# Optimization experiments

Measured on AMD Instinct MI355X. Metric: run time of the kernel, lower is better.

Reference implementation:

```python
import jax, jax.numpy as jnp
import numpy as np

N = 100000   # nodes
E = 1600000  # edges (before self-loops)
G = 64       # graphs in batch
IN = 8
H = 4        # heads
EPS_BN = 1e-5

def setup_inputs() -> dict:
    key = jax.random.key(0)
    ks = jax.random.split(key, 30)
    def nrm(k, shape, s=0.1):
        return jax.random.normal(k, shape, dtype=jnp.float32) * s
    inp = {}
    inp['x'] = nrm(ks[0], (N, IN), 1.0)
    inp['edge_index'] = jax.random.randint(ks[1], (2, E), 0, N)
    inp['batch'] = jnp.sort(jax.random.randint(ks[2], (N,), 0, G))
    # GATConv 1: 8 -> 64, 4 heads (concat=False)
    inp['W1'] = nrm(ks[3], (IN, H * 64)); inp['aS1'] = nrm(ks[4], (H, 64)); inp['aD1'] = nrm(ks[5], (H, 64)); inp['b1'] = jnp.zeros((64,), jnp.float32)
    inp['g1'] = jnp.ones((64,), jnp.float32); inp['be1'] = jnp.zeros((64,), jnp.float32)
    # GATConv 2: 64 -> 64
    inp['W2'] = nrm(ks[6], (64, H * 64)); inp['aS2'] = nrm(ks[7], (H, 64)); inp['aD2'] = nrm(ks[8], (H, 64)); inp['b2'] = jnp.zeros((64,), jnp.float32)
    inp['g2'] = jnp.ones((64,), jnp.float32); inp['be2'] = jnp.zeros((64,), jnp.float32)
    # GATConv 3: 64 -> 32
    inp['W3'] = nrm(ks[9], (64, H * 32)); inp['aS3'] = nrm(ks[10], (H, 32)); inp['aD3'] = nrm(ks[11], (H, 32)); inp['b3'] = jnp.zeros((32,), jnp.float32)
    inp['g3'] = jnp.ones((32,), jnp.float32); inp['be3'] = jnp.zeros((32,), jnp.float32)
    # predictor MLP 32 -> 16 -> 1
    inp['Wp1'] = nrm(ks[12], (32, 16)); inp['bp1'] = jnp.zeros((16,), jnp.float32)
    inp['Wp2'] = nrm(ks[13], (16, 1)); inp['bp2'] = jnp.zeros((1,), jnp.float32)
    return inp

def gat_layer(x, src, dst, W, a_src, a_dst, bias, D):
    # x: [N, Fin]; src/dst: [E'] (self-loops included). PyG GATConv semantics.
    h = (x @ W).reshape(N, H, D)                       # [N,H,D]
    alpha_s = jnp.einsum('nhd,hd->nh', h, a_src)       # [N,H]
    alpha_d = jnp.einsum('nhd,hd->nh', h, a_dst)
    e = jax.nn.leaky_relu(alpha_s[src] + alpha_d[dst], 0.2)  # [E',H]
    # segment softmax over incoming edges of each target node
    m = jax.ops.segment_max(e, dst, num_segments=N)
    e = jnp.exp(e - m[dst])
    s = jax.ops.segment_sum(e, dst, num_segments=N)
    alpha = e / (s[dst] + 1e-16)                       # [E',H]
    out = jax.ops.segment_sum(h[src] * alpha[:, :, None], dst, num_segments=N)  # [N,H,D]
    return out.mean(axis=1) + bias                     # concat=False -> head mean

def batch_norm(x, gamma, beta):
    m = x.mean(0)
    v = x.var(0)
    return (x - m) * jax.lax.rsqrt(v + EPS_BN) * gamma + beta

def reference(x, edge_index, batch,
              W1, aS1, aD1, b1, g1, be1,
              W2, aS2, aD2, b2, g2, be2,
              W3, aS3, aD3, b3, g3, be3,
              Wp1, bp1, Wp2, bp2):
    loop = jnp.arange(N)
    src = jnp.concatenate([edge_index[0], loop])  # add self loops (PyG default)
    dst = jnp.concatenate([edge_index[1], loop])
    h = jax.nn.relu(gat_layer(x, src, dst, W1, aS1, aD1, b1, 64))
    h = batch_norm(h, g1, be1)
    h = jax.nn.relu(gat_layer(h, src, dst, W2, aS2, aD2, b2, 64))
    h = batch_norm(h, g2, be2)
    h = jax.nn.relu(gat_layer(h, src, dst, W3, aS3, aD3, b3, 32))
    h = batch_norm(h, g3, be3)
    # global mean pool over graphs
    cnt = jax.ops.segment_sum(jnp.ones((N,), h.dtype), batch, num_segments=G)
    pooled = jax.ops.segment_sum(h, batch, num_segments=G) / jnp.maximum(cnt, 1.0)[:, None]
    hid = jax.nn.relu(pooled @ Wp1 + bp1)
    return hid @ Wp2 + bp2  # [G,1]
```

## Files before the change

kernel.cpp:

```cpp
#include <hip/hip_runtime.h>
#include <hip/hip_fp16.h>

#define N_NODES 100000
#define N_EDGES 1600000
#define EP (N_EDGES + N_NODES)
#define NG 64
#define NH 4
#define POOL_NPB 256
#define BSHIFT 7
#define BNODES 128
#define NBUCK 782
#define BCAP 3072
#define BCHUNK 4096
#define NBLK2 (N_NODES / 16)
#define NBLK1 (N_NODES / 32)

static inline int cdiv(int a, int b) { return (a + b - 1) / b; }

typedef _Float16 half8 __attribute__((ext_vector_type(8)));
typedef float f32x4 __attribute__((ext_vector_type(4)));

__device__ __forceinline__ float lrelu(float x) { return x >= 0.f ? x : 0.2f * x; }

__global__ __launch_bounds__(256) void k_bucket(const int* __restrict__ ei,
                                                int* __restrict__ gCursor,
                                                unsigned int* __restrict__ pairs) {
  __shared__ int cnt[NBUCK];
  __shared__ int base[NBUCK];
  int tid = threadIdx.x;
  for (int b = tid; b < NBUCK; b += 256) cnt[b] = 0;
  __syncthreads();
  int e0 = blockIdx.x * BCHUNK;
  unsigned int stV[16];
  int stB[16];
#pragma unroll
  for (int i = 0; i < 16; i++) {
    int e = e0 + i * 256 + tid;
    stB[i] = -1;
    if (e < EP) {
      int d, s;
      if (e < N_EDGES) {
        d = __builtin_nontemporal_load(&ei[N_EDGES + e]);
        s = __builtin_nontemporal_load(&ei[e]);
      } else {
        d = s = e - N_EDGES;
      }
      int b = d >> BSHIFT;
      stV[i] = ((unsigned int)s << BSHIFT) | (unsigned int)(d & (BNODES - 1));
      stB[i] = b;
      atomicAdd(&cnt[b], 1);
    }
  }
  __syncthreads();
  for (int b = tid; b < NBUCK; b += 256) {
    base[b] = atomicAdd(&gCursor[b], cnt[b]);
    cnt[b] = 0;
  }
  __syncthreads();
#pragma unroll
  for (int i = 0; i < 16; i++) {
    if (stB[i] >= 0) {
      int r = atomicAdd(&cnt[stB[i]], 1);
      pairs[base[stB[i]] + r] = stV[i];
    }
  }
}

__global__ __launch_bounds__(1024) void k_bscan(const int* __restrict__ gCursor,
                                                int* __restrict__ bstart) {
  __shared__ int sh[1024];
  int t = threadIdx.x;
  int v = (t < NBUCK) ? (gCursor[t] - t * BCAP) : 0;
  sh[t] = v;
  __syncthreads();
  for (int off = 1; off < 1024; off <<= 1) {
    int add = (t >= off) ? sh[t - off] : 0;
    __syncthreads();
    sh[t] += add;
    __syncthreads();
  }
  if (t < NBUCK) {
    bstart[t] = sh[t] - v;
    if (t == NBUCK - 1) bstart[NBUCK] = sh[t];
  }
}

__global__ __launch_bounds__(256) void k_build(const unsigned int* __restrict__ pairs,
                                               const int* __restrict__ bstart,
                                               int* __restrict__ indptr, int* __restrict__ esrc) {
  __shared__ int cnt[BNODES];
  __shared__ int exc[BNODES];
  __shared__ int ptr[BNODES];
  __shared__ int eLds[BCAP];
  int b = blockIdx.x;
  int tid = threadIdx.x;
  int obase = bstart[b];
  int nE = bstart[b + 1] - obase;
  int pbase = b * BCAP;
  if (tid < BNODES) cnt[tid] = 0;
  __syncthreads();
  unsigned int stV[12];
#pragma unroll
  for (int i = 0; i < 12; i++) {
    int idx = i * 256 + tid;
    stV[i] = 0xFFFFFFFFu;
    if (idx < nE) {
      unsigned int v = pairs[pbase + idx];
      stV[i] = v;
      atomicAdd(&cnt[v & (BNODES - 1)], 1);
    }
  }
  __syncthreads();
  if (tid < BNODES) ptr[tid] = cnt[tid];
  __syncthreads();
  for (int off = 1; off < BNODES; off <<= 1) {
    int add = (tid < BNODES && tid >= off) ? ptr[tid - off] : 0;
    __syncthreads();
    if (tid < BNODES) ptr[tid] += add;
    __syncthreads();
  }
  if (tid < BNODES) {
    exc[tid] = ptr[tid] - cnt[tid];
    int n = (b << BSHIFT) + tid;
    if (n < N_NODES) indptr[n] = obase + exc[tid];
    cnt[tid] = 0;
  }
  if (b == NBUCK - 1 && tid == 0) indptr[N_NODES] = bstart[NBUCK];
  __syncthreads();
#pragma unroll
  for (int i = 0; i < 12; i++) {
    if (stV[i] != 0xFFFFFFFFu) {
      int ln = stV[i] & (BNODES - 1);
      int r = atomicAdd(&cnt[ln], 1);
      eLds[exc[ln] + r] = (int)(stV[i] >> BSHIFT);
    }
  }
  __syncthreads();
  for (int idx = tid; idx < nE; idx += 256) esrc[obase + idx] = eLds[idx];
}

template <int FIN, int D>
__device__ void wvec_impl(const float* __restrict__ W, const float* __restrict__ aS,
                          const float* __restrict__ aD, float* __restrict__ wS,
                          float* __restrict__ wD, int t) {
  if (t >= 4 * FIN) return;
  int h = t / FIN, k = t % FIN;
  float ss = 0.f, dd = 0.f;
  for (int d = 0; d < D; d++) {
    float w = W[k * (4 * D) + h * D + d];
    ss = fmaf(w, aS[h * D + d], ss);
    dd = fmaf(w, aD[h * D + d], dd);
  }
  wS[h * FIN + k] = ss;
  wD[h * FIN + k] = dd;
}

template <int D>
__device__ void wcvt_frag(const float* __restrict__ W, __half* __restrict__ wf, int frag, int l) {
  constexpr int NCT = D / 16;
  int kt = frag / NCT, ct = frag % NCT;
  half8 v;
#pragma unroll
  for (int j = 0; j < 8; j++) {
    int kk = kt * 32 + (l >> 4) * 8 + j;
    int k = kk >> 2, h = kk & 3;
    v[j] = (_Float16)W[k * (4 * D) + h * D + ct * 16 + (l & 15)];
  }
  *(half8*)(wf + (size_t)frag * 512 + l * 8) = v;
}

__global__ __launch_bounds__(256) void k_prep(const float* W1, const float* aS1, const float* aD1,
                                              const float* W2, const float* aS2, const float* aD2,
                                              const float* W3, const float* aS3, const float* aD3,
                                              float* wS1, float* wD1, float* wS2, float* wD2,
                                              float* wS3, float* wD3,
                                              __half* wf1, __half* wf2, __half* wf3,
                                              int* gCursor) {
  int b = blockIdx.x, t = threadIdx.x;
  int f = t >> 6, l = t & 63;
  if (b == 0) wvec_impl<8, 64>(W1, aS1, aD1, wS1, wD1, t);
  else if (b == 1) wvec_impl<64, 64>(W2, aS2, aD2, wS2, wD2, t);
  else if (b == 2) wvec_impl<64, 32>(W3, aS3, aD3, wS3, wD3, t);
  else if (b == 3) wcvt_frag<64>(W1, wf1, f, l);
  else if (b < 12) wcvt_frag<64>(W2, wf2, (b - 4) * 4 + f, l);
  else if (b < 16) wcvt_frag<32>(W3, wf3, (b - 12) * 4 + f, l);
  else {
    int idx = (b - 16) * 256 + t;
    if (idx < NBUCK) gCursor[idx] = idx * BCAP;
  }
}

__global__ void k_attdots1(const float* __restrict__ x, const float* __restrict__ wS,
                           const float* __restrict__ wD, float4* __restrict__ as4,
                           float4* __restrict__ ad4) {
  int n = blockIdx.x * blockDim.x + threadIdx.x;
  if (n >= N_NODES) return;
  float4 s = {0, 0, 0, 0}, d = {0, 0, 0, 0};
#pragma unroll
  for (int k = 0; k < 8; k++) {
    float xv = x[(size_t)n * 8 + k];
    s.x = fmaf(xv, wS[k], s.x);
    s.y = fmaf(xv, wS[8 + k], s.y);
    s.z = fmaf(xv, wS[16 + k], s.z);
    s.w = fmaf(xv, wS[24 + k], s.w);
    d.x = fmaf(xv, wD[k], d.x);
    d.y = fmaf(xv, wD[8 + k], d.y);
    d.z = fmaf(xv, wD[16 + k], d.z);
    d.w = fmaf(xv, wD[24 + k], d.w);
  }
  as4[n] = s;
  ad4[n] = d;
}

__global__ __launch_bounds__(256) void k_bnx(const float* __restrict__ tbuf,
                                             const float* __restrict__ scale,
                                             const float* __restrict__ shift,
                                             const float* __restrict__ wS,
                                             const float* __restrict__ wD,
                                             __half* __restrict__ xhat,
                                             float4* __restrict__ as4, float4* __restrict__ ad4) {
  int lane = threadIdx.x & 63;
  int n = blockIdx.x * 4 + (threadIdx.x >> 6);
  if (n >= N_NODES) return;
  float v = fmaf(tbuf[(size_t)n * 64 + lane], scale[lane], shift[lane]);
  xhat[(size_t)n * 64 + lane] = __float2half(v);
  float p0 = v * wS[lane], p1 = v * wS[64 + lane], p2 = v * wS[128 + lane], p3 = v * wS[192 + lane];
  float q0 = v * wD[lane], q1 = v * wD[64 + lane], q2 = v * wD[128 + lane], q3 = v * wD[192 + lane];
#pragma unroll
  for (int off = 32; off; off >>= 1) {
    p0 += __shfl_xor(p0, off); p1 += __shfl_xor(p1, off);
    p2 += __shfl_xor(p2, off); p3 += __shfl_xor(p3, off);
    q0 += __shfl_xor(q0, off); q1 += __shfl_xor(q1, off);
    q2 += __shfl_xor(q2, off); q3 += __shfl_xor(q3, off);
  }
  if (lane == 0) {
    as4[n] = make_float4(p0, p1, p2, p3);
    ad4[n] = make_float4(q0, q1, q2, q3);
  }
}

__global__ __launch_bounds__(256) void k_aggp1(const int* __restrict__ indptr,
                                               const int* __restrict__ esrc,
                                               const float* __restrict__ xg,
                                               const float4* __restrict__ as4,
                                               const float4* __restrict__ ad4,
                                               const __half* __restrict__ wfrag,
                                               const float* __restrict__ bias,
                                               float* __restrict__ tbuf,
                                               float* __restrict__ part) {
  constexpr int GL = 8, NPW = 8, WB = NPW * (GL + 1);
  __shared__ int sOff[4 * WB];
  __shared__ float4 sW[4 * WB];
  __shared__ __align__(16) __half aT[32 * 40];
  int tid = threadIdx.x;
  int lane = tid & 63;
  int wv = tid >> 6;
  int q = lane & 7;
  int g = lane >> 3;
  int row = wv * 8 + g;
  int n = blockIdx.x * 32 + row;
  int e0 = indptr[n], e1 = indptr[n + 1];
  float4 ad = ad4[n];
  int lbase = wv * WB + g * (GL + 1);
  const char* xb = (const char*)xg + q * 4;
  float s0 = 0.f, s1 = 0.f, s2 = 0.f, s3 = 0.f;
  float a0 = 0.f, a1 = 0.f, a2 = 0.f, a3 = 0.f;
  for (int c = e0; c < e1; c += GL) {
    int nc = min(GL, e1 - c);
    float w0 = 0.f, w1 = 0.f, w2 = 0.f, w3 = 0.f;
    int sB = 0;
    if (q < nc) {
      int sidx = esrc[c + q];
      float4 av = as4[sidx];
      w0 = __expf(lrelu(av.x + ad.x));
      w1 = __expf(lrelu(av.y + ad.y));
      w2 = __expf(lrelu(av.z + ad.z));
      w3 = __expf(lrelu(av.w + ad.w));
      sB = sidx << 5;
    }
    s0 += w0; s1 += w1; s2 += w2; s3 += w3;
    sOff[lbase + q] = sB;
    sW[lbase + q] = make_float4(w0, w1, w2, w3);
    __builtin_amdgcn_wave_barrier();
    for (int i = 0; i < nc; ++i) {
      float4 w = sW[lbase + i];
      float xv = *(const float*)(xb + sOff[lbase + i]);
      a0 = fmaf(w.x, xv, a0);
      a1 = fmaf(w.y, xv, a1);
      a2 = fmaf(w.z, xv, a2);
      a3 = fmaf(w.w, xv, a3);
    }
    __builtin_amdgcn_wave_barrier();
  }
#pragma unroll
  for (int off = 1; off < GL; off <<= 1) {
    s0 += __shfl_xor(s0, off);
    s1 += __shfl_xor(s1, off);
    s2 += __shfl_xor(s2, off);
    s3 += __shfl_xor(s3, off);
  }
  float r0 = 1.f / (s0 + 1e-16f), r1 = 1.f / (s1 + 1e-16f);
  float r2 = 1.f / (s2 + 1e-16f), r3 = 1.f / (s3 + 1e-16f);
  __half2 p01 = __floats2half2_rn(a0 * r0, a1 * r1);
  __half2 p23 = __floats2half2_rn(a2 * r2, a3 * r3);
  uint2 pk = make_uint2(*(unsigned*)&p01, *(unsigned*)&p23);
  *(uint2*)&aT[row * 40 + q * 4] = pk;
  __syncthreads();
  int ct = wv;
  int m = lane & 15, kg = lane >> 4;
  half8 bv = *(const half8*)(wfrag + ((size_t)ct * 64 + lane) * 8);
  float bvs = bias[ct * 16 + m];
  float psum = 0.f, psq = 0.f;
#pragma unroll
  for (int tt = 0; tt < 2; tt++) {
    half8 avf = *(const half8*)&aT[(tt * 16 + m) * 40 + kg * 8];
    f32x4 cacc = (f32x4){0.f, 0.f, 0.f, 0.f};
    cacc = __builtin_amdgcn_mfma_f32_16x16x32_f16(avf, bv, cacc, 0, 0, 0);
#pragma unroll
    for (int j = 0; j < 4; j++) {
      int nr = blockIdx.x * 32 + tt * 16 + kg * 4 + j;
      float ov = fmaxf(fmaf(cacc[j], 0.25f, bvs), 0.f);
      tbuf[(size_t)nr * 64 + ct * 16 + m] = ov;
      psum += ov;
      psq = fmaf(ov, ov, psq);
    }
  }
  psum += __shfl_xor(psum, 16); psum += __shfl_xor(psum, 32);
  psq += __shfl_xor(psq, 16); psq += __shfl_xor(psq, 32);
  if (kg == 0) {
    part[(size_t)blockIdx.x * 128 + ct * 16 + m] = psum;
    part[(size_t)blockIdx.x * 128 + 64 + ct * 16 + m] = psq;
  }
}

template <int DOUT>
__global__ __launch_bounds__(256) void k_aggp(const int* __restrict__ indptr,
                                              const int* __restrict__ esrc,
                                              const __half* __restrict__ xg,
                                              const float4* __restrict__ as4,
                                              const float4* __restrict__ ad4,
                                              const __half* __restrict__ wfrag,
                                              const float* __restrict__ bias,
                                              float* __restrict__ tbuf,
                                              float* __restrict__ part) {
  constexpr int NCT = DOUT / 16;
  constexpr int GL = 16, NPW = 4, WB = NPW * (GL + 1);
  __shared__ int sOff[4 * WB];
  __shared__ float4 sW[4 * WB];
  __shared__ __align__(16) __half aT[16 * 264];
  int tid = threadIdx.x;
  int lane = tid & 63;
  int wv = tid >> 6;
  int q = lane & 15;
  int g = lane >> 4;
  int row = wv * 4 + g;
  int n = blockIdx.x * 16 + row;
  int e0 = indptr[n], e1 = indptr[n + 1];
  float4 ad = ad4[n];
  int lbase = wv * WB + g * (GL + 1);
  const char* xb = (const char*)xg + q * 8;
  float s0 = 0.f, s1 = 0.f, s2 = 0.f, s3 = 0.f;
  float a[4][4];
#pragma unroll
  for (int d = 0; d < 4; d++)
#pragma unroll
    for (int h = 0; h < 4; h++) a[d][h] = 0.f;

  for (int c = e0; c < e1; c += GL) {
    int nc = min(GL, e1 - c);
    float w0 = 0.f, w1 = 0.f, w2 = 0.f, w3 = 0.f;
    int sB = 0;
    if (q < nc) {
      int sidx = esrc[c + q];
      float4 av = as4[sidx];
      w0 = __expf(lrelu(av.x + ad.x));
      w1 = __expf(lrelu(av.y + ad.y));
      w2 = __expf(lrelu(av.z + ad.z));
      w3 = __expf(lrelu(av.w + ad.w));
      sB = sidx << 7;
    }
    s0 += w0; s1 += w1; s2 += w2; s3 += w3;
    sOff[lbase + q] = sB;
    sW[lbase + q] = make_float4(w0, w1, w2, w3);
    __builtin_amdgcn_wave_barrier();
    for (int i = 0; i < nc; ++i) {
      float4 w = sW[lbase + i];
      uint2 px = *(const uint2*)(xb + sOff[lbase + i]);
      float2 f01 = __half22float2(*(const __half2*)&px.x);
      float2 f23 = __half22float2(*(const __half2*)&px.y);
      a[0][0] = fmaf(w.x, f01.x, a[0][0]); a[0][1] = fmaf(w.y, f01.x, a[0][1]);
      a[0][2] = fmaf(w.z, f01.x, a[0][2]); a[0][3] = fmaf(w.w, f01.x, a[0][3]);
      a[1][0] = fmaf(w.x, f01.y, a[1][0]); a[1][1] = fmaf(w.y, f01.y, a[1][1]);
      a[1][2] = fmaf(w.z, f01.y, a[1][2]); a[1][3] = fmaf(w.w, f01.y, a[1][3]);
      a[2][0] = fmaf(w.x, f23.x, a[2][0]); a[2][1] = fmaf(w.y, f23.x, a[2][1]);
      a[2][2] = fmaf(w.z, f23.x, a[2][2]); a[2][3] = fmaf(w.w, f23.x, a[2][3]);
      a[3][0] = fmaf(w.x, f23.y, a[3][0]); a[3][1] = fmaf(w.y, f23.y, a[3][1]);
      a[3][2] = fmaf(w.z, f23.y, a[3][2]); a[3][3] = fmaf(w.w, f23.y, a[3][3]);
    }
    __builtin_amdgcn_wave_barrier();
  }
#pragma unroll
  for (int off = 1; off < GL; off <<= 1) {
    s0 += __shfl_xor(s0, off);
    s1 += __shfl_xor(s1, off);
    s2 += __shfl_xor(s2, off);
    s3 += __shfl_xor(s3, off);
  }
  float r0 = 1.f / (s0 + 1e-16f), r1 = 1.f / (s1 + 1e-16f);
  float r2 = 1.f / (s2 + 1e-16f), r3 = 1.f / (s3 + 1e-16f);
  __half2 p[8];
#pragma unroll
  for (int d = 0; d < 4; d++) {
    p[2 * d] = __floats2half2_rn(a[d][0] * r0, a[d][1] * r1);
    p[2 * d + 1] = __floats2half2_rn(a[d][2] * r2, a[d][3] * r3);
  }
  uint4 lo = make_uint4(*(unsigned*)&p[0], *(unsigned*)&p[1], *(unsigned*)&p[2], *(unsigned*)&p[3]);
  uint4 hi = make_uint4(*(unsigned*)&p[4], *(unsigned*)&p[5], *(unsigned*)&p[6], *(unsigned*)&p[7]);
  *(uint4*)&aT[row * 264 + q * 16] = lo;
  *(uint4*)&aT[row * 264 + q * 16 + 8] = hi;
  __syncthreads();
  if (wv < NCT) {
    int ct = wv;
    int m = lane & 15, kg = lane >> 4;
    f32x4 cacc = (f32x4){0.f, 0.f, 0.f, 0.f};
#pragma unroll
    for (int kt = 0; kt < 8; kt++) {
      half8 avf = *(const half8*)&aT[m * 264 + kt * 32 + kg * 8];
      half8 bvf = *(const half8*)(wfrag + ((kt * NCT + ct) * 64 + lane) * 8);
      cacc = __builtin_amdgcn_mfma_f32_16x16x32_f16(avf, bvf, cacc, 0, 0, 0);
    }
    float bv = bias[ct * 16 + m];
    float psum = 0.f, psq = 0.f;
#pragma unroll
    for (int j = 0; j < 4; j++) {
      int nr = blockIdx.x * 16 + kg * 4 + j;
      float ov = fmaxf(fmaf(cacc[j], 0.25f, bv), 0.f);
      tbuf[(size_t)nr * DOUT + ct * 16 + m] = ov;
      psum += ov;
      psq = fmaf(ov, ov, psq);
    }
    psum += __shfl_xor(psum, 16); psum += __shfl_xor(psum, 32);
    psq += __shfl_xor(psq, 16); psq += __shfl_xor(psq, 32);
    if (kg == 0) {
      part[(size_t)blockIdx.x * (2 * DOUT) + ct * 16 + m] = psum;
      part[(size_t)blockIdx.x * (2 * DOUT) + DOUT + ct * 16 + m] = psq;
    }
  }
}

template <int C>
__global__ __launch_bounds__(256) void k_bnfin2(const float* __restrict__ part, int nb,
                                                const float* __restrict__ g,
                                                const float* __restrict__ be,
                                                float* __restrict__ scale,
                                                float* __restrict__ shift) {
  int c = blockIdx.x;
  int t = threadIdx.x;
  float s = 0.f, q = 0.f;
  for (int b = t; b < nb; b += 256) {
    s += part[(size_t)b * (2 * C) + c];
    q += part[(size_t)b * (2 * C) + C + c];
  }
  __shared__ float sh[512];
  sh[t] = s;
  sh[256 + t] = q;
  __syncthreads();
  for (int step = 128; step; step >>= 1) {
    if (t < step) {
      sh[t] += sh[t + step];
      sh[256 + t] += sh[256 + t + step];
    }
    __syncthreads();
  }
  if (t == 0) {
    float mean = sh[0] / (float)N_NODES;
    float var = sh[256] / (float)N_NODES - mean * mean;
    float sc = g[c] * rsqrtf(var + 1e-5f);
    scale[c] = sc;
    shift[c] = be[c] - mean * sc;
  }
}

__global__ __launch_bounds__(256) void k_pool(const float* __restrict__ f3,
                                              const int* __restrict__ batch,
                                              const float* __restrict__ scale,
                                              const float* __restrict__ shift,
                                              float* __restrict__ pool,
                                              float* __restrict__ cntg) {
  __shared__ float acc[NG][33];
  int t = threadIdx.x;
  for (int i = t; i < NG * 33; i += 256) ((float*)acc)[i] = 0.f;
  __syncthreads();
  int c = t & 31, rg = t >> 5;
  float sc = scale[c], sh = shift[c];
  int n0 = blockIdx.x * POOL_NPB;
  int n1 = min(N_NODES, n0 + POOL_NPB);
  float r = 0.f, rc = 0.f;
  int gcur = -1;
  for (int n = n0 + rg; n < n1; n += 8) {
    int g = batch[n];
    if (g != gcur) {
      if (gcur >= 0) {
        atomicAdd(&acc[gcur][c], r);
        if (c == 0) atomicAdd(&acc[gcur][32], rc);
      }
      gcur = g;
      r = 0.f;
      rc = 0.f;
    }
    r += fmaf(f3[(size_t)n * 32 + c], sc, sh);
    rc += 1.f;
  }
  if (gcur >= 0) {
    atomicAdd(&acc[gcur][c], r);
    if (c == 0) atomicAdd(&acc[gcur][32], rc);
  }
  __syncthreads();
  for (int i = t; i < NG * 32; i += 256) {
    int g = i >> 5, cc = i & 31;
    float v = acc[g][cc];
    if (v != 0.f) atomicAdd(&pool[i], v);
  }
  for (int g = t; g < NG; g += 256) {
    float v = acc[g][32];
    if (v != 0.f) atomicAdd(&cntg[g], v);
  }
}

__global__ void k_mlp(const float* __restrict__ pool, const float* __restrict__ cntg,
                      const float* __restrict__ Wp1, const float* __restrict__ bp1,
                      const float* __restrict__ Wp2, const float* __restrict__ bp2,
                      float* __restrict__ out) {
  int g = threadIdx.x;
  if (g >= NG) return;
  float inv = 1.f / fmaxf(cntg[g], 1.f);
  float p[32];
#pragma unroll
  for (int c = 0; c < 32; c++) p[c] = pool[g * 32 + c] * inv;
  float o = bp2[0];
  for (int j = 0; j < 16; j++) {
    float hsum = bp1[j];
#pragma unroll
    for (int c = 0; c < 32; c++) hsum = fmaf(p[c], Wp1[c * 16 + j], hsum);
    o = fmaf(fmaxf(hsum, 0.f), Wp2[j], o);
  }
  out[g] = o;
}

extern "C" void kernel_launch(void* const* d_in, const int* in_sizes, int n_in,
                              void* d_out, int out_size, void* d_ws, size_t ws_size,
                              hipStream_t stream) {
  const float* x = (const float*)d_in[0];
  const int* ei = (const int*)d_in[1];
  const int* batch = (const int*)d_in[2];
  const float* W1 = (const float*)d_in[3];
  const float* aS1 = (const float*)d_in[4];
  const float* aD1 = (const float*)d_in[5];
  const float* b1 = (const float*)d_in[6];
  const float* g1 = (const float*)d_in[7];
  const float* be1 = (const float*)d_in[8];
  const float* W2 = (const float*)d_in[9];
  const float* aS2 = (const float*)d_in[10];
  const float* aD2 = (const float*)d_in[11];
  const float* b2 = (const float*)d_in[12];
  const float* g2 = (const float*)d_in[13];
  const float* be2 = (const float*)d_in[14];
  const float* W3 = (const float*)d_in[15];
  const float* aS3 = (const float*)d_in[16];
  const float* aD3 = (const float*)d_in[17];
  const float* b3 = (const float*)d_in[18];
  const float* g3 = (const float*)d_in[19];
  const float* be3 = (const float*)d_in[20];
  const float* Wp1 = (const float*)d_in[21];
  const float* bp1 = (const float*)d_in[22];
  const float* Wp2 = (const float*)d_in[23];
  const float* bp2 = (const float*)d_in[24];
  float* out = (float*)d_out;

  size_t off = 0;
  auto alloc = [&](size_t bytes) -> void* {
    void* p = (char*)d_ws + off;
    off += (bytes + 255) & ~(size_t)255;
    return p;
  };
  float* pool = (float*)alloc((size_t)NG * 32 * 4);
  float* cntg = (float*)alloc((size_t)NG * 4);
  size_t zbytes = off;
  int* gCursor = (int*)alloc((size_t)NBUCK * 4);
  int* bstart = (int*)alloc((size_t)(NBUCK + 1) * 4);
  unsigned int* pairs = (unsigned int*)alloc((size_t)NBUCK * BCAP * 4);
  int* indptr = (int*)alloc((size_t)(N_NODES + 1) * 4);
  int* esrc = (int*)alloc((size_t)EP * 4);
  __half* xhat = (__half*)alloc((size_t)N_NODES * 64 * 2);
  float* as_ = (float*)alloc((size_t)N_NODES * 16);
  float* ad_ = (float*)alloc((size_t)N_NODES * 16);
  float* tbuf = (float*)alloc((size_t)N_NODES * 64 * 4);
  float* part = (float*)alloc((size_t)NBLK2 * 128 * 4);
  float* scale = (float*)alloc(64 * 4);
  float* shift = (float*)alloc(64 * 4);
  float* wS1 = (float*)alloc(32 * 4);
  float* wD1 = (float*)alloc(32 * 4);
  float* wS2 = (float*)alloc(256 * 4);
  float* wD2 = (float*)alloc(256 * 4);
  float* wS3 = (float*)alloc(256 * 4);
  float* wD3 = (float*)alloc(256 * 4);
  __half* wf1 = (__half*)alloc((size_t)4 * 512 * 2);
  __half* wf2 = (__half*)alloc((size_t)32 * 512 * 2);
  __half* wf3 = (__half*)alloc((size_t)16 * 512 * 2);
  if (off > ws_size) return;

  hipMemsetAsync(pool, 0, zbytes, stream);

  k_prep<<<16 + cdiv(NBUCK, 256), 256, 0, stream>>>(W1, aS1, aD1, W2, aS2, aD2, W3, aS3, aD3,
                                                    wS1, wD1, wS2, wD2, wS3, wD3, wf1, wf2, wf3,
                                                    gCursor);
  k_bucket<<<cdiv(EP, BCHUNK), 256, 0, stream>>>(ei, gCursor, pairs);
  k_bscan<<<1, 1024, 0, stream>>>(gCursor, bstart);
  k_build<<<NBUCK, 256, 0, stream>>>(pairs, bstart, indptr, esrc);

  k_attdots1<<<cdiv(N_NODES, 256), 256, 0, stream>>>(x, wS1, wD1, (float4*)as_, (float4*)ad_);
  k_aggp1<<<NBLK1, 256, 0, stream>>>(indptr, esrc, x, (const float4*)as_,
                                     (const float4*)ad_, wf1, b1, tbuf, part);
  k_bnfin2<64><<<64, 256, 0, stream>>>(part, NBLK1, g1, be1, scale, shift);

  k_bnx<<<cdiv(N_NODES, 4), 256, 0, stream>>>(tbuf, scale, shift, wS2, wD2, xhat,
                                              (float4*)as_, (float4*)ad_);
  k_aggp<64><<<NBLK2, 256, 0, stream>>>(indptr, esrc, xhat, (const float4*)as_,
                                        (const float4*)ad_, wf2, b2, tbuf, part);
  k_bnfin2<64><<<64, 256, 0, stream>>>(part, NBLK2, g2, be2, scale, shift);

  k_bnx<<<cdiv(N_NODES, 4), 256, 0, stream>>>(tbuf, scale, shift, wS3, wD3, xhat,
                                              (float4*)as_, (float4*)ad_);
  k_aggp<32><<<NBLK2, 256, 0, stream>>>(indptr, esrc, xhat, (const float4*)as_,
                                        (const float4*)ad_, wf3, b3, tbuf, part);
  k_bnfin2<32><<<32, 256, 0, stream>>>(part, NBLK2, g3, be3, scale, shift);

  k_pool<<<cdiv(N_NODES, POOL_NPB), 256, 0, stream>>>(tbuf, batch, scale, shift, pool, cntg);
  k_mlp<<<1, 64, 0, stream>>>(pool, cntg, Wp1, bp1, Wp2, bp2, out);
}
```

Measured before the change: 382.4 us.

## Sort nodes by degree for balanced aggregation and fold batch-norm into aggregation

Builds a degree histogram during CSR construction, then scans and scatters it into a degree-sorted node permutation. The aggregation kernels process nodes in that order, so nodes in the same wave have similar edge counts and less divergence. Layer outputs are now stored as fp16 and the batch-norm affine is applied inside the next aggregation, so k_dots only computes attention dots and the separate normalized-feature buffer is dropped. This adds two small kernels and scattered (permuted) output writes, and stores intermediates in half precision.

```diff
diff --git a/kernel.cpp b/kernel.cpp
--- a/kernel.cpp
+++ b/kernel.cpp
@@ -14,6 +14,7 @@
 #define BCHUNK 4096
 #define NBLK2 (N_NODES / 16)
 #define NBLK1 (N_NODES / 32)
+#define NBINS 64
 
 static inline int cdiv(int a, int b) { return (a + b - 1) / b; }
 
@@ -87,10 +88,12 @@
 
 __global__ __launch_bounds__(256) void k_build(const unsigned int* __restrict__ pairs,
                                                const int* __restrict__ bstart,
-                                               int* __restrict__ indptr, int* __restrict__ esrc) {
+                                               int* __restrict__ indptr, int* __restrict__ esrc,
+                                               int* __restrict__ ghist) {
   __shared__ int cnt[BNODES];
   __shared__ int exc[BNODES];
   __shared__ int ptr[BNODES];
+  __shared__ int dh[NBINS];
   __shared__ int eLds[BCAP];
   int b = blockIdx.x;
   int tid = threadIdx.x;
@@ -98,6 +101,7 @@
   int nE = bstart[b + 1] - obase;
   int pbase = b * BCAP;
   if (tid < BNODES) cnt[tid] = 0;
+  if (tid >= BNODES && tid < BNODES + NBINS) dh[tid - BNODES] = 0;
   __syncthreads();
   unsigned int stV[12];
 #pragma unroll
@@ -122,11 +126,15 @@
   if (tid < BNODES) {
     exc[tid] = ptr[tid] - cnt[tid];
     int n = (b << BSHIFT) + tid;
-    if (n < N_NODES) indptr[n] = obase + exc[tid];
+    if (n < N_NODES) {
+      indptr[n] = obase + exc[tid];
+      atomicAdd(&dh[min(cnt[tid], NBINS - 1)], 1);
+    }
     cnt[tid] = 0;
   }
   if (b == NBUCK - 1 && tid == 0) indptr[N_NODES] = bstart[NBUCK];
   __syncthreads();
+  if (tid < NBINS && dh[tid]) atomicAdd(&ghist[tid], dh[tid]);
 #pragma unroll
   for (int i = 0; i < 12; i++) {
     if (stV[i] != 0xFFFFFFFFu) {
@@ -137,6 +145,51 @@
   }
   __syncthreads();
   for (int idx = tid; idx < nE; idx += 256) esrc[obase + idx] = eLds[idx];
+}
+
+__global__ void k_dscan(const int* __restrict__ ghist, int* __restrict__ binCur) {
+  if (threadIdx.x == 0) {
+    int acc = 0;
+    for (int b = 0; b < NBINS; b++) {
+      binCur[b] = acc;
+      acc += ghist[b];
+    }
+  }
+}
+
+__global__ __launch_bounds__(256) void k_dscat(const int* __restrict__ indptr,
+                                               int* __restrict__ binCur,
+                                               int* __restrict__ perm) {
+  __shared__ int cnt[NBINS];
+  __shared__ int base[NBINS];
+  int t = threadIdx.x;
+  if (t < NBINS) cnt[t] = 0;
+  __syncthreads();
+  int binr[2], nr[2];
+#pragma unroll
+  for (int i = 0; i < 2; i++) {
+    int n = blockIdx.x * 512 + i * 256 + t;
+    binr[i] = -1;
+    if (n < N_NODES) {
+      int deg = indptr[n + 1] - indptr[n];
+      binr[i] = min(deg, NBINS - 1);
+      nr[i] = n;
+      atomicAdd(&cnt[binr[i]], 1);
+    }
+  }
+  __syncthreads();
+  if (t < NBINS) {
+    base[t] = cnt[t] ? atomicAdd(&binCur[t], cnt[t]) : 0;
+    cnt[t] = 0;
+  }
+  __syncthreads();
+#pragma unroll
+  for (int i = 0; i < 2; i++) {
+    if (binr[i] >= 0) {
+      int r = atomicAdd(&cnt[binr[i]], 1);
+      perm[base[binr[i]] + r] = nr[i];
+    }
+  }
 }
 
 template <int FIN, int D>
@@ -212,18 +265,16 @@
   ad4[n] = d;
 }
 
-__global__ __launch_bounds__(256) void k_bnx(const float* __restrict__ tbuf,
-                                             const float* __restrict__ scale,
-                                             const float* __restrict__ shift,
-                                             const float* __restrict__ wS,
-                                             const float* __restrict__ wD,
-                                             __half* __restrict__ xhat,
-                                             float4* __restrict__ as4, float4* __restrict__ ad4) {
+__global__ __launch_bounds__(256) void k_dots(const __half* __restrict__ t16,
+                                              const float* __restrict__ scale,
+                                              const float* __restrict__ shift,
+                                              const float* __restrict__ wS,
+                                              const float* __restrict__ wD,
+                                              float4* __restrict__ as4, float4* __restrict__ ad4) {
   int lane = threadIdx.x & 63;
   int n = blockIdx.x * 4 + (threadIdx.x >> 6);
   if (n >= N_NODES) return;
-  float v = fmaf(tbuf[(size_t)n * 64 + lane], scale[lane], shift[lane]);
-  xhat[(size_t)n * 64 + lane] = __float2half(v);
+  float v = fmaf(__half2float(t16[(size_t)n * 64 + lane]), scale[lane], shift[lane]);
   float p0 = v * wS[lane], p1 = v * wS[64 + lane], p2 = v * wS[128 + lane], p3 = v * wS[192 + lane];
   float q0 = v * wD[lane], q1 = v * wD[64 + lane], q2 = v * wD[128 + lane], q3 = v * wD[192 + lane];
 #pragma unroll
@@ -240,13 +291,14 @@
 }
 
 __global__ __launch_bounds__(256) void k_aggp1(const int* __restrict__ indptr,
+                                               const int* __restrict__ perm,
                                                const int* __restrict__ esrc,
                                                const float* __restrict__ xg,
                                                const float4* __restrict__ as4,
                                                const float4* __restrict__ ad4,
                                                const __half* __restrict__ wfrag,
                                                const float* __restrict__ bias,
-                                               float* __restrict__ tbuf,
+                                               __half* __restrict__ out16,
                                                float* __restrict__ part) {
   constexpr int GL = 8, NPW = 8, WB = NPW * (GL + 1);
   __shared__ int sOff[4 * WB];
@@ -258,7 +310,7 @@
   int q = lane & 7;
   int g = lane >> 3;
   int row = wv * 8 + g;
-  int n = blockIdx.x * 32 + row;
+  int n = perm[blockIdx.x * 32 + row];
   int e0 = indptr[n], e1 = indptr[n + 1];
   float4 ad = ad4[n];
   int lbase = wv * WB + g * (GL + 1);
@@ -318,9 +370,9 @@
     cacc = __builtin_amdgcn_mfma_f32_16x16x32_f16(avf, bv, cacc, 0, 0, 0);
 #pragma unroll
     for (int j = 0; j < 4; j++) {
-      int nr = blockIdx.x * 32 + tt * 16 + kg * 4 + j;
+      int nr = perm[blockIdx.x * 32 + tt * 16 + kg * 4 + j];
       float ov = fmaxf(fmaf(cacc[j], 0.25f, bvs), 0.f);
-      tbuf[(size_t)nr * 64 + ct * 16 + m] = ov;
+      out16[(size_t)nr * 64 + ct * 16 + m] = __float2half(ov);
       psum += ov;
       psq = fmaf(ov, ov, psq);
     }
@@ -333,15 +385,19 @@
   }
 }
 
-template <int DOUT>
+template <int DOUT, bool OUTH>
 __global__ __launch_bounds__(256) void k_aggp(const int* __restrict__ indptr,
+                                              const int* __restrict__ perm,
                                               const int* __restrict__ esrc,
                                               const __half* __restrict__ xg,
                                               const float4* __restrict__ as4,
                                               const float4* __restrict__ ad4,
                                               const __half* __restrict__ wfrag,
                                               const float* __restrict__ bias,
-                                              float* __restrict__ tbuf,
+                                              const float* __restrict__ scale,
+                                              const float* __restrict__ shift,
+                                              __half* __restrict__ out16,
+                                              float* __restrict__ out32,
                                               float* __restrict__ part) {
   constexpr int NCT = DOUT / 16;
   constexpr int GL = 16, NPW = 4, WB = NPW * (GL + 1);
@@ -354,7 +410,7 @@
   int q = lane & 15;
   int g = lane >> 4;
   int row = wv * 4 + g;
-  int n = blockIdx.x * 16 + row;
+  int n = perm[blockIdx.x * 16 + row];
   int e0 = indptr[n], e1 = indptr[n + 1];
   float4 ad = ad4[n];
   int lbase = wv * WB + g * (GL + 1);
@@ -411,8 +467,9 @@
   __half2 p[8];
 #pragma unroll
   for (int d = 0; d < 4; d++) {
-    p[2 * d] = __floats2half2_rn(a[d][0] * r0, a[d][1] * r1);
-    p[2 * d + 1] = __floats2half2_rn(a[d][2] * r2, a[d][3] * r3);
+    float sc = scale[q * 4 + d], sh = shift[q * 4 + d];
+    p[2 * d] = __floats2half2_rn(fmaf(a[d][0] * r0, sc, sh), fmaf(a[d][1] * r1, sc, sh));
+    p[2 * d + 1] = __floats2half2_rn(fmaf(a[d][2] * r2, sc, sh), fmaf(a[d][3] * r3, sc, sh));
   }
   uint4 lo = make_uint4(*(unsigned*)&p[0], *(unsigned*)&p[1], *(unsigned*)&p[2], *(unsigned*)&p[3]);
   uint4 hi = make_uint4(*(unsigned*)&p[4], *(unsigned*)&p[5], *(unsigned*)&p[6], *(unsigned*)&p[7]);
@@ -433,9 +490,10 @@
     float psum = 0.f, psq = 0.f;
 #pragma unroll
     for (int j = 0; j < 4; j++) {
-      int nr = blockIdx.x * 16 + kg * 4 + j;
+      int nr = perm[blockIdx.x * 16 + kg * 4 + j];
       float ov = fmaxf(fmaf(cacc[j], 0.25f, bv), 0.f);
-      tbuf[(size_t)nr * DOUT + ct * 16 + m] = ov;
+      if constexpr (OUTH) out16[(size_t)nr * DOUT + ct * 16 + m] = __float2half(ov);
+      else out32[(size_t)nr * DOUT + ct * 16 + m] = ov;
       psum += ov;
       psq = fmaf(ov, ov, psq);
     }
@@ -585,16 +643,20 @@
   };
   float* pool = (float*)alloc((size_t)NG * 32 * 4);
   float* cntg = (float*)alloc((size_t)NG * 4);
+  int* ghist = (int*)alloc((size_t)NBINS * 4);
   size_t zbytes = off;
   int* gCursor = (int*)alloc((size_t)NBUCK * 4);
   int* bstart = (int*)alloc((size_t)(NBUCK + 1) * 4);
   unsigned int* pairs = (unsigned int*)alloc((size_t)NBUCK * BCAP * 4);
   int* indptr = (int*)alloc((size_t)(N_NODES + 1) * 4);
   int* esrc = (int*)alloc((size_t)EP * 4);
-  __half* xhat = (__half*)alloc((size_t)N_NODES * 64 * 2);
+  int* perm = (int*)alloc((size_t)N_NODES * 4);
+  int* binCur = (int*)alloc((size_t)NBINS * 4);
+  __half* t16a = (__half*)alloc((size_t)N_NODES * 64 * 2);
+  __half* t16b = (__half*)alloc((size_t)N_NODES * 64 * 2);
   float* as_ = (float*)alloc((size_t)N_NODES * 16);
   float* ad_ = (float*)alloc((size_t)N_NODES * 16);
-  float* tbuf = (float*)alloc((size_t)N_NODES * 64 * 4);
+  float* tbuf = (float*)alloc((size_t)N_NODES * 32 * 4);
   float* part = (float*)alloc((size_t)NBLK2 * 128 * 4);
   float* scale = (float*)alloc(64 * 4);
   float* shift = (float*)alloc(64 * 4);
@@ -616,23 +678,27 @@
                                                     gCursor);
   k_bucket<<<cdiv(EP, BCHUNK), 256, 0, stream>>>(ei, gCursor, pairs);
   k_bscan<<<1, 1024, 0, stream>>>(gCursor, bstart);
-  k_build<<<NBUCK, 256, 0, stream>>>(pairs, bstart, indptr, esrc);
+  k_build<<<NBUCK, 256, 0, stream>>>(pairs, bstart, indptr, esrc, ghist);
+  k_dscan<<<1, 64, 0, stream>>>(ghist, binCur);
+  k_dscat<<<cdiv(N_NODES, 512), 256, 0, stream>>>(indptr, binCur, perm);
 
   k_attdots1<<<cdiv(N_NODES, 256), 256, 0, stream>>>(x, wS1, wD1, (float4*)as_, (float4*)ad_);
-  k_aggp1<<<NBLK1, 256, 0, stream>>>(indptr, esrc, x, (const float4*)as_,
-                                     (const float4*)ad_, wf1, b1, tbuf, part);
+  k_aggp1<<<NBLK1, 256, 0, stream>>>(indptr, perm, esrc, x, (const float4*)as_,
+                                     (const float4*)ad_, wf1, b1, t16a, part);
   k_bnfin2<64><<<64, 256, 0, stream>>>(part, NBLK1, g1, be1, scale, shift);
 
-  k_bnx<<<cdiv(N_NODES, 4), 256, 0, stream>>>(tbuf, scale, shift, wS2, wD2, xhat,
-                                              (float4*)as_, (float4*)ad_);
-  k_aggp<64><<<NBLK2, 256, 0, stream>>>(indptr, esrc, xhat, (const float4*)as_,
-                                        (const float4*)ad_, wf2, b2, tbuf, part);
+  k_dots<<<cdiv(N_NODES, 4), 256, 0, stream>>>(t16a, scale, shift, wS2, wD2,
+                                               (float4*)as_, (float4*)ad_);
+  k_aggp<64, true><<<NBLK2, 256, 0, stream>>>(indptr, perm, esrc, t16a, (const float4*)as_,
+                                              (const float4*)ad_, wf2, b2, scale, shift,
+                                              t16b, nullptr, part);
   k_bnfin2<64><<<64, 256, 0, stream>>>(part, NBLK2, g2, be2, scale, shift);
 
-  k_bnx<<<cdiv(N_NODES, 4), 256, 0, stream>>>(tbuf, scale, shift, wS3, wD3, xhat,
-                                              (float4*)as_, (float4*)ad_);
-  k_aggp<32><<<NBLK2, 256, 0, stream>>>(indptr, esrc, xhat, (const float4*)as_,
-                                        (const float4*)ad_, wf3, b3, tbuf, part);
+  k_dots<<<cdiv(N_NODES, 4), 256, 0, stream>>>(t16b, scale, shift, wS3, wD3,
+                                               (float4*)as_, (float4*)ad_);
+  k_aggp<32, false><<<NBLK2, 256, 0, stream>>>(indptr, perm, esrc, t16b, (const float4*)as_,
+                                               (const float4*)ad_, wf3, b3, scale, shift,
+                                               nullptr, tbuf, part);
   k_bnfin2<32><<<32, 256, 0, stream>>>(part, NBLK2, g3, be3, scale, shift);
 
   k_pool<<<cdiv(N_NODES, POOL_NPB), 256, 0, stream>>>(tbuf, batch, scale, shift, pool, cntg);
```

Result: no change. 377.6 us (-1.3%).
